# Kernel optimization log

Hardware: AMD Instinct MI355X
Metric: run time of the kernel (lower is better)

The kernel has to match this reference:

```python
import jax, jax.numpy as jnp
import numpy as np

H1, W1 = 16, 16  # SparseAttBlock stride
EPS = 1e-5       # BatchNorm eps


def _att(x, wx, bx, wy, by, wo, bo, gamma, beta):
    """DotProductAttBlock: 1x1 q/k projections, full softmax attention over
    the H*W tokens of each (small) block, then 1x1 conv + BatchNorm(train) + ReLU."""
    B, C, H, W = x.shape
    xf = x.reshape(B, C, H * W)                                  # [B,C,N]
    theta = jnp.einsum('mc,bcn->bnm', wx, xf) + bx               # [B,N,fmid]
    psi = jnp.einsum('mc,bcn->bmn', wy, xf) + by[:, None]        # [B,fmid,N]
    alpha = jax.nn.softmax(jnp.einsum('bnm,bmk->bnk', theta, psi), axis=2)  # [B,N,N]
    agg = jnp.einsum('bnk,bck->bcn', alpha, xf)                  # [B,C,N]
    out = jnp.einsum('oc,bcn->bon', wo, agg) + bo[:, None]       # [B,fout,N]
    # BatchNorm2d in training mode: biased batch stats over (batch, spatial)
    mean = out.mean(axis=(0, 2), keepdims=True)
    var = ((out - mean) ** 2).mean(axis=(0, 2), keepdims=True)
    out = (out - mean) * jax.lax.rsqrt(var + EPS) * gamma[:, None] + beta[:, None]
    return jax.nn.relu(out).reshape(B, -1, H, W)


def _forward(x, p1, p2):
    B, C, H, W = x.shape
    h2, w2 = H // H1, W // W1
    # pass 1: attention within each (H1,W1) block, blocks folded into batch
    xb = x.reshape(B, C, H1, h2, W1, w2).transpose(0, 3, 5, 1, 2, 4)
    xb = xb.reshape(B * h2 * w2, C, H1, W1)
    xb = _att(xb, *p1)
    # pass 2: attention across the (h2,w2) block grid
    xb = xb.reshape(B, h2, w2, C, H1, W1).transpose(0, 4, 5, 3, 1, 2)
    xb = xb.reshape(B * H1 * W1, C, h2, w2)
    xb = _att(xb, *p2)
    return xb.reshape(B, H1, W1, C, h2, w2).transpose(0, 3, 1, 4, 2, 5).reshape(B, C, H, W)


def setup_inputs() -> dict:
    key = jax.random.key(0)
    ks = jax.random.split(key, 20)
    B, C, FMID, H, W = 4, 128, 64, 256, 256
    s = 0.05
    d = {'x': jax.random.normal(ks[0], (B, C, H, W), jnp.float32)}
    d['w1x'] = jax.random.normal(ks[1], (FMID, C), jnp.float32) * s
    d['b1x'] = jax.random.normal(ks[2], (FMID,), jnp.float32) * s
    d['w1y'] = jax.random.normal(ks[3], (FMID, C), jnp.float32) * s
    d['b1y'] = jax.random.normal(ks[4], (FMID,), jnp.float32) * s
    d['w1o'] = jax.random.normal(ks[5], (C, C), jnp.float32) * s
    d['b1o'] = jax.random.normal(ks[6], (C,), jnp.float32) * s
    d['g1'] = jnp.ones((C,), jnp.float32)
    d['be1'] = jnp.zeros((C,), jnp.float32)
    d['w2x'] = jax.random.normal(ks[7], (FMID, C), jnp.float32) * s
    d['b2x'] = jax.random.normal(ks[8], (FMID,), jnp.float32) * s
    d['w2y'] = jax.random.normal(ks[9], (FMID, C), jnp.float32) * s
    d['b2y'] = jax.random.normal(ks[10], (FMID,), jnp.float32) * s
    d['w2o'] = jax.random.normal(ks[11], (C, C), jnp.float32) * s
    d['b2o'] = jax.random.normal(ks[12], (C,), jnp.float32) * s
    d['g2'] = jnp.ones((C,), jnp.float32)
    d['be2'] = jnp.zeros((C,), jnp.float32)
    return d


def reference(x, w1x, b1x, w1y, b1y, w1o, b1o, g1, be1,
              w2x, b2x, w2y, b2y, w2o, b2o, g2, be2):
    p1 = (w1x, b1x, w1y, b1y, w1o, b1o, g1, be1)
    p2 = (w2x, b2x, w2y, b2y, w2o, b2o, g2, be2)
    return _forward(x, p1, p2)
```

## Files before the change

### kernel.cpp

```cpp
#include <hip/hip_runtime.h>

typedef _Float16 f16;
typedef f16 f16x2 __attribute__((ext_vector_type(2)));
typedef f16 f16x4 __attribute__((ext_vector_type(4)));
typedef f16 f16x8 __attribute__((ext_vector_type(8)));
typedef float f32x4 __attribute__((ext_vector_type(4)));
typedef float f32x16 __attribute__((ext_vector_type(16)));
typedef unsigned int u32;
typedef u32 u32x2 __attribute__((ext_vector_type(2)));
typedef u32 u32x4 __attribute__((ext_vector_type(4)));

#define MFMA32(a, b, c) __builtin_amdgcn_mfma_f32_32x32x16_f16((a), (b), (c), 0, 0, 0)

__device__ __forceinline__ u32 pk2(float a, float b) {
    return __builtin_bit_cast(u32, __builtin_amdgcn_cvt_pkrtz(a, b));
}
__device__ __forceinline__ f16x4 lo4(f16x8 v) { return __builtin_shufflevector(v, v, 0, 1, 2, 3); }
__device__ __forceinline__ f16x4 hi4(f16x8 v) { return __builtin_shufflevector(v, v, 4, 5, 6, 7); }

__device__ __forceinline__ f16x8 xfrm(f32x16 v, int rb) {
    u32 a0 = pk2(v[rb + 0], v[rb + 1]);
    u32 a1 = pk2(v[rb + 2], v[rb + 3]);
    u32 b0 = pk2(v[rb + 4], v[rb + 5]);
    u32 b1 = pk2(v[rb + 6], v[rb + 7]);
    u32x2 r0 = __builtin_amdgcn_permlane32_swap(a0, b0, false, false);
    u32x2 r1 = __builtin_amdgcn_permlane32_swap(a1, b1, false, false);
    u32x4 aw = {r0.x, r1.x, r0.y, r1.y};
    return __builtin_bit_cast(f16x8, aw);
}
__device__ __forceinline__ f16x8 add8(f16x8 a, f16x8 b) {
    f16x8 r;
#pragma unroll
    for (int j = 0; j < 8; ++j) r[j] = a[j] + b[j];
    return r;
}

#define AD_OFF_Y 65536
#define AD_OFF_V 98304
#define AD_LDS   163840

#define WSTRIDE 32896

__global__ __launch_bounds__(512) void repack_kernel(const float* __restrict__ x,
                                                     f16* __restrict__ Xall) {
    __shared__ f16 XT[128 * 264];
    const int tid = threadIdx.x, g = blockIdx.x;
    const int b = g >> 8, i1 = (g >> 4) & 15, i2 = g & 15;
    const int h = i1 * 16 + i2;
    {
        const int c = tid >> 2, wq = (tid & 3) * 64;
        const float* src = x + (((size_t)b * 128 + c) * 256 + h) * 256 + wq;
        f16* dst = XT + c * 264 + wq;
#pragma unroll
        for (int i = 0; i < 16; ++i) {
            f32x4 v = *(const f32x4*)(src + i * 4);
            f16x4 o = {(f16)v[0], (f16)v[1], (f16)v[2], (f16)v[3]};
            *(f16x4*)(dst + i * 4) = o;
        }
    }
    __syncthreads();
    {
        const int w = tid >> 1, ch = (tid & 1) * 64;
        const int j1 = w >> 4, j2 = w & 15;
        f16* dst = Xall + (((size_t)b * 256 + i2 * 16 + j2) * 256 + i1 * 16 + j1) * 128 + ch;
#pragma unroll
        for (int i = 0; i < 8; ++i) {
            f16x8 v;
#pragma unroll
            for (int j = 0; j < 8; ++j) v[j] = XT[(ch + i * 8 + j) * 264 + w];
            *(f16x8*)(dst + i * 8) = v;
        }
    }
}

__global__ void wconv_kernel(const float* __restrict__ w1x, const float* __restrict__ w1y,
                             const float* __restrict__ w1o, const float* __restrict__ b1x,
                             const float* __restrict__ b1y, const float* __restrict__ w2x,
                             const float* __restrict__ w2y, const float* __restrict__ w2o,
                             const float* __restrict__ b2x, const float* __restrict__ b2y,
                             f16* __restrict__ Wf, float* __restrict__ gstats) {
    int i = blockIdx.x * 256 + threadIdx.x;
    if (i < 65536) {
        int p = i >> 15, idx = i & 32767;
        int j = idx & 7, lane = (idx >> 3) & 63, ks = (idx >> 9) & 7, r = idx >> 12;
        int row = r * 32 + (lane & 31);
        int c = ks * 16 + (lane >> 5) * 8 + j;
        const float* s;
        if (p == 0) s = (row < 128) ? w1o + row * 128 : (row < 192) ? w1x + (row - 128) * 128
                                                                   : w1y + (row - 192) * 128;
        else        s = (row < 128) ? w2o + row * 128 : (row < 192) ? w2x + (row - 128) * 128
                                                                   : w2y + (row - 192) * 128;
        Wf[p * WSTRIDE + idx] = (f16)s[c];
    } else if (i < 65792) {
        int idx2 = i - 65536;
        int p = idx2 >> 7, r = idx2 & 127;
        const float* bsrc = (p == 0) ? ((r < 64) ? b1x : b1y) : ((r < 64) ? b2x : b2y);
        Wf[p * WSTRIDE + 32768 + r] = (f16)bsrc[r & 63];
    } else {
        gstats[i - 65792] = 0.f;
    }
}

template <int PASS>
__global__ __launch_bounds__(512, 2) void attd_kernel(
    const f16* __restrict__ Xin, const f16* __restrict__ Wf, const float* __restrict__ bo,
    const float* __restrict__ bnab, f16* __restrict__ Uout, float* __restrict__ gstats,
    int t_stride, int s_stride) {
    __shared__ __align__(16) char smem[AD_LDS];
    const int tid = threadIdx.x;
    const int w = tid >> 6, l = tid & 63, hl = l >> 5, l31 = l & 31;
    const int g = blockIdx.x, R0 = w * 32;

    const f16* bfp = Wf + 32768;
    f16x8 bqf[4], bkf[4];
#pragma unroll
    for (int ks = 0; ks < 4; ++ks) {
        bqf[ks] = *(const f16x8*)(bfp + ks * 16 + hl * 8);
        bkf[ks] = *(const f16x8*)(bfp + 64 + ks * 16 + hl * 8);
    }
    float bov[4];
#pragma unroll
    for (int ct = 0; ct < 4; ++ct) bov[ct] = bo[ct * 32 + l31];

    f16x8 afr[8];
    {
        f16x8 wv[8];
#pragma unroll
        for (int j = 0; j < 8; ++j)
            wv[j] = *(const f16x8*)((const char*)Wf + (j * 512 + tid) * 16);
        const f16* src = Xin + (size_t)g * 32768 + (R0 + l31) * 128 + hl * 8;
#pragma unroll
        for (int ks = 0; ks < 8; ++ks) afr[ks] = *(const f16x8*)(src + ks * 16);
        if constexpr (PASS == 2) {
#pragma unroll
            for (int ks = 0; ks < 8; ++ks) {
                const int c0 = ks * 16 + hl * 8;
                f32x4 a0 = *(const f32x4*)(bnab + c0), a1 = *(const f32x4*)(bnab + c0 + 4);
                f32x4 s0 = *(const f32x4*)(bnab + 128 + c0), s1 = *(const f32x4*)(bnab + 132 + c0);
                f16x8 v = afr[ks];
#pragma unroll
                for (int j = 0; j < 4; ++j) {
                    v[j]     = (f16)fmaxf(a0[j] * (float)v[j]     + s0[j], 0.f);
                    v[j + 4] = (f16)fmaxf(a1[j] * (float)v[j + 4] + s1[j], 0.f);
                }
                afr[ks] = v;
            }
        }
#pragma unroll
        for (int j = 0; j < 8; ++j)
            *(f16x8*)(smem + (j * 512 + tid) * 16) = wv[j];
    }
    __syncthreads();

    {
        f32x16 aP[2] = {};
#pragma unroll
        for (int ks = 0; ks < 8; ++ks)
#pragma unroll
            for (int mt = 0; mt < 2; ++mt) {
                f16x8 wk = *(const f16x8*)(smem + (((6 + mt) * 8 + ks) * 64 + l) * 16);
                aP[mt] = MFMA32(wk, afr[ks], aP[mt]);
            }
#pragma unroll
        for (int ks = 0; ks < 4; ++ks) {
            f16x8 yf = add8(xfrm(aP[ks >> 1], 8 * (ks & 1)), bkf[ks]);
            *(f16x8*)(smem + AD_OFF_Y + ((w * 4 + ks) * 64 + l) * 16) = yf;
        }
    }

    f16x8 tb[4];
    {
        f32x16 aT[2] = {};
#pragma unroll
        for (int ks = 0; ks < 8; ++ks)
#pragma unroll
            for (int mt = 0; mt < 2; ++mt) {
                f16x8 wq = *(const f16x8*)(smem + (((4 + mt) * 8 + ks) * 64 + l) * 16);
                aT[mt] = MFMA32(wq, afr[ks], aT[mt]);
            }
#pragma unroll
        for (int ks = 0; ks < 4; ++ks)
            tb[ks] = add8(xfrm(aT[ks >> 1], 8 * (ks & 1)), bqf[ks]);
    }

    {
        f32x16 aV[4] = {};
#pragma unroll
        for (int ks = 0; ks < 8; ++ks)
#pragma unroll
            for (int ct = 0; ct < 4; ++ct) {
                f16x8 wo = *(const f16x8*)(smem + ((ct * 8 + ks) * 64 + l) * 16);
                aV[ct] = MFMA32(afr[ks], wo, aV[ct]);
            }
#pragma unroll
        for (int ct = 0; ct < 4; ++ct) {
#pragma unroll
            for (int e = 0; e < 16; ++e) aV[ct][e] += bov[ct];
#pragma unroll
            for (int ksl = 0; ksl < 2; ++ksl)
                *(f16x8*)(smem + AD_OFF_V + (((2 * w + ksl) * 4 + ct) * 64 + l) * 16) =
                    xfrm(aV[ct], 8 * ksl);
        }
    }
    __syncthreads();

    f32x16 s[8] = {};
    __builtin_amdgcn_s_setprio(1);
#pragma unroll
    for (int kt = 0; kt < 8; ++kt)
#pragma unroll
        for (int ks = 0; ks < 4; ++ks) {
            f16x8 ay = *(const f16x8*)(smem + AD_OFF_Y + ((kt * 4 + ks) * 64 + l) * 16);
            s[kt] = MFMA32(ay, tb[ks], s[kt]);
        }
    __builtin_amdgcn_s_setprio(0);

    float mx = -1e30f;
#pragma unroll
    for (int kt = 0; kt < 8; ++kt) {
        float m0 = fmaxf(fmaxf(s[kt][0], s[kt][1]), fmaxf(s[kt][2], s[kt][3]));
        float m1 = fmaxf(fmaxf(s[kt][4], s[kt][5]), fmaxf(s[kt][6], s[kt][7]));
        float m2 = fmaxf(fmaxf(s[kt][8], s[kt][9]), fmaxf(s[kt][10], s[kt][11]));
        float m3 = fmaxf(fmaxf(s[kt][12], s[kt][13]), fmaxf(s[kt][14], s[kt][15]));
        mx = fmaxf(mx, fmaxf(fmaxf(m0, m1), fmaxf(m2, m3)));
    }
    mx = fmaxf(mx, __shfl_xor(mx, 32));
    float sum = 0.f;
#pragma unroll
    for (int kt = 0; kt < 8; ++kt)
#pragma unroll
        for (int e = 0; e < 16; ++e) {
            float p = __expf(s[kt][e] - mx);
            s[kt][e] = p;
            sum += p;
        }
    sum += __shfl_xor(sum, 32);
    const float rs = 1.f / sum;
#pragma unroll
    for (int kt = 0; kt < 8; ++kt)
#pragma unroll
        for (int e = 0; e < 16; ++e) s[kt][e] *= rs;

    f32x16 o[4] = {};
#pragma unroll
    for (int kt = 0; kt < 8; ++kt)
#pragma unroll
        for (int ks2 = 0; ks2 < 2; ++ks2) {
            f16x8 ap = xfrm(s[kt], 8 * ks2);
            __builtin_amdgcn_s_setprio(1);
#pragma unroll
            for (int ct = 0; ct < 4; ++ct) {
                f16x8 bv =
                    *(const f16x8*)(smem + AD_OFF_V + (((kt * 2 + ks2) * 4 + ct) * 64 + l) * 16);
                o[ct] = MFMA32(ap, bv, o[ct]);
            }
            __builtin_amdgcn_s_setprio(0);
        }

    float ssa[4], sqa[4];
#pragma unroll
    for (int ct = 0; ct < 4; ++ct) {
        float ss = 0.f, sq = 0.f;
#pragma unroll
        for (int e = 0; e < 16; ++e) {
            float v = o[ct][e];
            ss += v;
            sq += v * v;
        }
        ssa[ct] = ss + __shfl_xor(ss, 32);
        sqa[ct] = sq + __shfl_xor(sq, 32);
    }
    const size_t ub = (size_t)(g >> 8) * 8388608 + (size_t)(g & 255) * (size_t)s_stride;
#pragma unroll
    for (int r = 0; r < 16; ++r) {
        int trow = (r & 3) + 8 * (r >> 2) + 4 * hl;
        f16* rp = Uout + ub + (size_t)(R0 + trow) * (size_t)t_stride + l31;
#pragma unroll
        for (int ct = 0; ct < 4; ++ct) rp[ct * 32] = (f16)o[ct][r];
    }
    __syncthreads();

    float* SS = (float*)(smem + AD_OFF_Y);
    if (hl == 0) {
#pragma unroll
        for (int ct = 0; ct < 4; ++ct) {
            SS[w * 128 + ct * 32 + l31] = ssa[ct];
            SS[1024 + w * 128 + ct * 32 + l31] = sqa[ct];
        }
    }
    __syncthreads();
    if (tid < 256) {
        int c = tid & 127, which = tid >> 7;
        float acc = 0.f;
#pragma unroll
        for (int iw = 0; iw < 8; ++iw) acc += SS[which * 1024 + iw * 128 + c];
        atomicAdd(&gstats[which * 128 + c], acc);
    }
}

__global__ void bnfix_kernel(const float* __restrict__ gstats, const float* __restrict__ gamma,
                             const float* __restrict__ beta, float* __restrict__ ab) {
    int c = threadIdx.x;
    if (c < 128) {
        const float inv = 1.f / 262144.f;
        float mean = gstats[c] * inv;
        float var = gstats[128 + c] * inv - mean * mean;
        float rstd = rsqrtf(var + 1e-5f);
        float a = gamma[c] * rstd;
        ab[c] = a;
        ab[128 + c] = beta[c] - mean * a;
    }
}

__global__ __launch_bounds__(256) void final_kernel(const f16* __restrict__ U2,
                                                    const float* __restrict__ gst,
                                                    const float* __restrict__ gamma,
                                                    const float* __restrict__ beta,
                                                    float* __restrict__ out) {
    __shared__ f16 L[256 * 132];
    __shared__ float AB[256];
    const int tid = threadIdx.x, g = blockIdx.x;
    const int b = g >> 8, i1 = (g >> 4) & 15, j1 = g & 15;
    if (tid < 128) {
        const float inv = 1.f / 262144.f;
        float mean = gst[tid] * inv;
        float var = gst[128 + tid] * inv - mean * mean;
        float a = gamma[tid] * rsqrtf(var + 1e-5f);
        AB[tid] = a;
        AB[128 + tid] = beta[tid] - mean * a;
    }
    const f16* src = U2 + (size_t)g * 32768;
#pragma unroll
    for (int e = 0; e < 16; ++e) {
        int u = e * 2048 + tid * 8;
        int row = u >> 7, c0 = u & 127;
        f16x8 v = *(const f16x8*)(src + u);
        f16* dst = L + row * 132 + c0;
        *(f16x4*)dst = lo4(v);
        *(f16x4*)(dst + 4) = hi4(v);
    }
    __syncthreads();
    const int j2q = tid & 3, u0 = tid >> 2;
#pragma unroll 4
    for (int k = 0; k < 32; ++k) {
        int unit = u0 + k * 64;
        int c = unit & 127, i2 = unit >> 7;
        float a = AB[c], bb = AB[128 + c];
        f32x4 vv;
#pragma unroll
        for (int jj = 0; jj < 4; ++jj)
            vv[jj] = fmaxf(a * (float)L[(i2 * 16 + j2q * 4 + jj) * 132 + c] + bb, 0.f);
        *(f32x4*)(out + (((size_t)b * 128 + c) * 256 + i1 * 16 + i2) * 256 + j1 * 16 + j2q * 4) =
            vv;
    }
}

extern "C" void kernel_launch(void* const* d_in, const int* in_sizes, int n_in, void* d_out,
                              int out_size, void* d_ws, size_t ws_size, hipStream_t stream) {
    (void)in_sizes; (void)n_in; (void)out_size; (void)ws_size;
    const float* x = (const float*)d_in[0];
    const float* w1x = (const float*)d_in[1];
    const float* b1x = (const float*)d_in[2];
    const float* w1y = (const float*)d_in[3];
    const float* b1y = (const float*)d_in[4];
    const float* w1o = (const float*)d_in[5];
    const float* b1o = (const float*)d_in[6];
    const float* g1 = (const float*)d_in[7];
    const float* be1 = (const float*)d_in[8];
    const float* w2x = (const float*)d_in[9];
    const float* b2x = (const float*)d_in[10];
    const float* w2y = (const float*)d_in[11];
    const float* b2y = (const float*)d_in[12];
    const float* w2o = (const float*)d_in[13];
    const float* b2o = (const float*)d_in[14];
    const float* g2 = (const float*)d_in[15];
    const float* be2 = (const float*)d_in[16];

    f16* Xall = (f16*)d_out;
    f16* U1 = (f16*)((char*)d_out + 67108864);
    f16* U2 = (f16*)d_ws;
    f16* Wbf = (f16*)((char*)d_ws + 67108864);
    float* gstats = (float*)((char*)d_ws + 67108864 + 262144);
    float* bnab = gstats + 512;

    wconv_kernel<<<259, 256, 0, stream>>>(w1x, w1y, w1o, b1x, b1y, w2x, w2y, w2o, b2x, b2y, Wbf,
                                          gstats);
    repack_kernel<<<1024, 512, 0, stream>>>(x, Xall);

    attd_kernel<1><<<1024, 512, 0, stream>>>(Xall, Wbf, b1o, (const float*)nullptr, U1, gstats,
                                             32768, 128);
    bnfix_kernel<<<1, 128, 0, stream>>>(gstats, g1, be1, bnab);
    attd_kernel<2><<<1024, 512, 0, stream>>>(U1, Wbf + WSTRIDE, b2o, bnab, U2, gstats + 256, 128,
                                             32768);
    final_kernel<<<1024, 256, 0, stream>>>(U2, gstats + 256, g2, be2, (float*)d_out);
}
```

Baseline: 253.4 us.

## Fuse input repack into pass-1 attention kernel via LDS transpose

Removes the separate repack kernel and has the pass-1 attention kernel gather its block of the fp32 input directly. The kernel converts the input to fp16 and transposes it through shared memory before loading the MFMA fragments. This drops the write and re-read of the intermediate fp16 buffer and one launch. The block index is also remapped so neighbouring workgroups touch nearby input. The trade-off is scattered scalar strided global loads (one float per thread per element) and an extra barrier, which may lower achieved bandwidth.

```diff
diff --git a/kernel.cpp b/kernel.cpp
--- a/kernel.cpp
+++ b/kernel.cpp
@@ -38,40 +38,9 @@
 #define AD_OFF_Y 65536
 #define AD_OFF_V 98304
 #define AD_LDS   163840
+#define XS_PITCH 136
 
 #define WSTRIDE 32896
-
-__global__ __launch_bounds__(512) void repack_kernel(const float* __restrict__ x,
-                                                     f16* __restrict__ Xall) {
-    __shared__ f16 XT[128 * 264];
-    const int tid = threadIdx.x, g = blockIdx.x;
-    const int b = g >> 8, i1 = (g >> 4) & 15, i2 = g & 15;
-    const int h = i1 * 16 + i2;
-    {
-        const int c = tid >> 2, wq = (tid & 3) * 64;
-        const float* src = x + (((size_t)b * 128 + c) * 256 + h) * 256 + wq;
-        f16* dst = XT + c * 264 + wq;
-#pragma unroll
-        for (int i = 0; i < 16; ++i) {
-            f32x4 v = *(const f32x4*)(src + i * 4);
-            f16x4 o = {(f16)v[0], (f16)v[1], (f16)v[2], (f16)v[3]};
-            *(f16x4*)(dst + i * 4) = o;
-        }
-    }
-    __syncthreads();
-    {
-        const int w = tid >> 1, ch = (tid & 1) * 64;
-        const int j1 = w >> 4, j2 = w & 15;
-        f16* dst = Xall + (((size_t)b * 256 + i2 * 16 + j2) * 256 + i1 * 16 + j1) * 128 + ch;
-#pragma unroll
-        for (int i = 0; i < 8; ++i) {
-            f16x8 v;
-#pragma unroll
-            for (int j = 0; j < 8; ++j) v[j] = XT[(ch + i * 8 + j) * 264 + w];
-            *(f16x8*)(dst + i * 8) = v;
-        }
-    }
-}
 
 __global__ void wconv_kernel(const float* __restrict__ w1x, const float* __restrict__ w1y,
                              const float* __restrict__ w1o, const float* __restrict__ b1x,
@@ -103,13 +72,14 @@
 
 template <int PASS>
 __global__ __launch_bounds__(512, 2) void attd_kernel(
-    const f16* __restrict__ Xin, const f16* __restrict__ Wf, const float* __restrict__ bo,
-    const float* __restrict__ bnab, f16* __restrict__ Uout, float* __restrict__ gstats,
-    int t_stride, int s_stride) {
+    const float* __restrict__ xsrc, const f16* __restrict__ Xin, const f16* __restrict__ Wf,
+    const float* __restrict__ bo, const float* __restrict__ bnab, f16* __restrict__ Uout,
+    float* __restrict__ gstats, int t_stride, int s_stride) {
     __shared__ __align__(16) char smem[AD_LDS];
     const int tid = threadIdx.x;
     const int w = tid >> 6, l = tid & 63, hl = l >> 5, l31 = l & 31;
-    const int g = blockIdx.x, R0 = w * 32;
+    const int R0 = w * 32;
+    const int g = (PASS == 1) ? ((blockIdx.x & 7) * 128 + (blockIdx.x >> 3)) : blockIdx.x;
 
     const f16* bfp = Wf + 32768;
     f16x8 bqf[4], bkf[4];
@@ -128,10 +98,24 @@
 #pragma unroll
         for (int j = 0; j < 8; ++j)
             wv[j] = *(const f16x8*)((const char*)Wf + (j * 512 + tid) * 16);
-        const f16* src = Xin + (size_t)g * 32768 + (R0 + l31) * 128 + hl * 8;
-#pragma unroll
-        for (int ks = 0; ks < 8; ++ks) afr[ks] = *(const f16x8*)(src + ks * 16);
-        if constexpr (PASS == 2) {
+
+        if constexpr (PASS == 1) {
+            f16* XS = (f16*)(smem + AD_OFF_Y);
+            const int b = g >> 8, i2 = (g >> 4) & 15, j2 = g & 15;
+            const int j1 = tid & 15, cg = (tid >> 4) & 31;
+            const float* xb = xsrc + ((size_t)b * 128 + cg * 4) * 65536 + i2 * 256 + j1 * 16 + j2;
+#pragma unroll
+            for (int i1 = 0; i1 < 16; ++i1) {
+#pragma unroll
+                for (int cs = 0; cs < 4; ++cs) {
+                    float v = xb[(size_t)cs * 65536 + i1 * 4096];
+                    XS[(i1 * 16 + j1) * XS_PITCH + cg * 4 + cs] = (f16)v;
+                }
+            }
+        } else {
+            const f16* src = Xin + (size_t)g * 32768 + (R0 + l31) * 128 + hl * 8;
+#pragma unroll
+            for (int ks = 0; ks < 8; ++ks) afr[ks] = *(const f16x8*)(src + ks * 16);
 #pragma unroll
             for (int ks = 0; ks < 8; ++ks) {
                 const int c0 = ks * 16 + hl * 8;
@@ -151,6 +135,14 @@
             *(f16x8*)(smem + (j * 512 + tid) * 16) = wv[j];
     }
     __syncthreads();
+
+    if constexpr (PASS == 1) {
+        const f16* XS = (const f16*)(smem + AD_OFF_Y);
+#pragma unroll
+        for (int ks = 0; ks < 8; ++ks)
+            afr[ks] = *(const f16x8*)(XS + (R0 + l31) * XS_PITCH + ks * 16 + hl * 8);
+        __syncthreads();
+    }
 
     {
         f32x16 aP[2] = {};
@@ -376,7 +368,6 @@
     const float* g2 = (const float*)d_in[15];
     const float* be2 = (const float*)d_in[16];
 
-    f16* Xall = (f16*)d_out;
     f16* U1 = (f16*)((char*)d_out + 67108864);
     f16* U2 = (f16*)d_ws;
     f16* Wbf = (f16*)((char*)d_ws + 67108864);
@@ -385,12 +376,11 @@
 
     wconv_kernel<<<259, 256, 0, stream>>>(w1x, w1y, w1o, b1x, b1y, w2x, w2y, w2o, b2x, b2y, Wbf,
                                           gstats);
-    repack_kernel<<<1024, 512, 0, stream>>>(x, Xall);
-
-    attd_kernel<1><<<1024, 512, 0, stream>>>(Xall, Wbf, b1o, (const float*)nullptr, U1, gstats,
-                                             32768, 128);
+
+    attd_kernel<1><<<1024, 512, 0, stream>>>(x, (const f16*)nullptr, Wbf, b1o,
+                                             (const float*)nullptr, U1, gstats, 32768, 128);
     bnfix_kernel<<<1, 128, 0, stream>>>(gstats, g1, be1, bnab);
-    attd_kernel<2><<<1024, 512, 0, stream>>>(U1, Wbf + WSTRIDE, b2o, bnab, U2, gstats + 256, 128,
-                                             32768);
+    attd_kernel<2><<<1024, 512, 0, stream>>>((const float*)nullptr, U1, Wbf + WSTRIDE, b2o, bnab,
+                                             U2, gstats + 256, 128, 32768);
     final_kernel<<<1024, 256, 0, stream>>>(U2, gstats + 256, g2, be2, (float*)d_out);
 }
```

Result: slower. 310.8 us (+22.7%).
